# Kernel optimization log

Hardware: AMD Instinct MI355X
Metric: run time of the kernel (lower is better)

Reference implementation:

```python
import jax, jax.numpy as jnp
import numpy as np

BITS = 4
GROUP = 128
MAXQ = 2 ** BITS - 1  # 15 for asymmetric 4-bit


def round_ste(x):
    # straight-through rounding: round in fwd, identity in bwd
    return x + jax.lax.stop_gradient(jnp.round(x) - x)


def quant_weight(weight, v, min_scale, max_scale):
    """Groupwise asymmetric fake-quant (quantize + dequantize) of weight.

    weight: [O, I], v: [O, I] learnable rounding offsets,
    min_scale/max_scale: [O*I/GROUP] learnable min/max scales in [-1, 0].
    """
    O, I = weight.shape
    w = weight.reshape(-1, GROUP)          # [G, GROUP]
    vv = v.reshape(-1, GROUP)              # [G, GROUP]
    wmin_t = jnp.minimum(w.min(axis=1), 0.0)  # [G]
    wmax_t = jnp.maximum(w.max(axis=1), 0.0)  # [G]
    # forward clamps min/max scale into [-1, 0] before use
    wmin = wmin_t * (jnp.clip(min_scale, -1.0, 0.0) + 1.0)
    wmax = wmax_t * (jnp.clip(max_scale, -1.0, 0.0) + 1.0)
    degenerate = (wmin == 0.0) & (wmax == 0.0)
    wmin = jnp.where(degenerate, -1.0, wmin)
    wmax = jnp.where(degenerate, 1.0, wmax)
    # scale stored at fp16 precision (scale_dtype), then used in fp32 math
    scale = ((wmax - wmin) / MAXQ).astype(jnp.float16).astype(weight.dtype)  # [G]
    zp = round_ste(-wmin / scale)                                            # [G]
    int_w = round_ste(w / scale[:, None] + vv)                               # [G, GROUP]
    q = jnp.clip(int_w + zp[:, None], 0.0, float(MAXQ))
    wq = scale[:, None] * (q - zp[:, None])
    return wq.reshape(O, I)


def setup_inputs() -> dict:
    key = jax.random.key(0)
    k_x, k_w, k_b, k_v = jax.random.split(key, 4)
    O, I = 4096, 4096
    B, S = 2, 2048
    x = jax.random.normal(k_x, (B, S, I), dtype=jnp.float32)
    weight = jax.random.normal(k_w, (O, I), dtype=jnp.float32) * 0.02
    bias = jax.random.normal(k_b, (O,), dtype=jnp.float32) * 0.02
    value = jax.random.normal(k_v, (O, I), dtype=jnp.float32) * 0.1
    n_groups = O * I // GROUP
    min_scale = jnp.zeros((n_groups,), dtype=jnp.float32)
    max_scale = jnp.zeros((n_groups,), dtype=jnp.float32)
    return {"x": x, "weight": weight, "bias": bias, "value": value,
            "min_scale": min_scale, "max_scale": max_scale}


def reference(x, weight, bias, value, min_scale, max_scale):
    wq = quant_weight(weight, value, min_scale, max_scale)  # [O, I]
    # F.linear(x, weight_q, bias): x @ wq.T + bias
    return jnp.einsum('bsi,oi->bso', x, wq) + bias
```

## Files before the change

### kernel.cpp

```cpp
#include <hip/hip_runtime.h>
#include <hip/hip_bf16.h>
#include <hip/hip_fp16.h>
#include <stdint.h>

#define M_DIM 4096
#define N_DIM 4096
#define K_DIM 4096
#define GROUPSZ 128
#define MAXQ 15.0f

#define BM 256
#define BN 256
#define BK 64
#define T_TILES (K_DIM / BK)

typedef __attribute__((ext_vector_type(8))) short short8;
typedef __attribute__((ext_vector_type(4))) float f32x4;

__global__ __launch_bounds__(256) void quant_kernel(
    const float* __restrict__ weight, const float* __restrict__ value,
    const float* __restrict__ min_scale, const float* __restrict__ max_scale,
    __hip_bfloat16* __restrict__ wq)
{
    const int tid  = threadIdx.x;
    const int wave = tid >> 6;
    const int lane = tid & 63;
    const long g    = (long)blockIdx.x * 4 + wave;
    const long base = g * GROUPSZ + lane * 2;

    const float2 w = *(const float2*)(weight + base);
    const float2 v = *(const float2*)(value  + base);

    float mn = fminf(w.x, w.y);
    float mx = fmaxf(w.x, w.y);
#pragma unroll
    for (int off = 32; off >= 1; off >>= 1) {
        mn = fminf(mn, __shfl_xor(mn, off, 64));
        mx = fmaxf(mx, __shfl_xor(mx, off, 64));
    }
    mn = fminf(mn, 0.0f);
    mx = fmaxf(mx, 0.0f);

    const float ms = fminf(fmaxf(min_scale[g], -1.0f), 0.0f) + 1.0f;
    const float xs = fminf(fmaxf(max_scale[g], -1.0f), 0.0f) + 1.0f;
    float wmin = mn * ms;
    float wmax = mx * xs;
    if (wmin == 0.0f && wmax == 0.0f) { wmin = -1.0f; wmax = 1.0f; }

    const float scale = (float)(_Float16)((wmax - wmin) / MAXQ);
    const float zp    = rintf(-wmin / scale);

    const float q0 = fminf(fmaxf(rintf(w.x / scale + v.x) + zp, 0.0f), MAXQ);
    const float q1 = fminf(fmaxf(rintf(w.y / scale + v.y) + zp, 0.0f), MAXQ);
    const float o0 = scale * (q0 - zp);
    const float o1 = scale * (q1 - zp);

    __hip_bfloat162 o;
    o.x = __float2bfloat16(o0);
    o.y = __float2bfloat16(o1);
    *(__hip_bfloat162*)(wq + base) = o;
}

__global__ __launch_bounds__(256) void cast_kernel(
    const float* __restrict__ x, __hip_bfloat16* __restrict__ xb)
{
    const long i = ((long)blockIdx.x * 256 + threadIdx.x) * 8;
    const float4 a = *(const float4*)(x + i);
    const float4 b = *(const float4*)(x + i + 4);
    union { short8 s; __hip_bfloat16 h[8]; } u;
    u.h[0] = __float2bfloat16(a.x);
    u.h[1] = __float2bfloat16(a.y);
    u.h[2] = __float2bfloat16(a.z);
    u.h[3] = __float2bfloat16(a.w);
    u.h[4] = __float2bfloat16(b.x);
    u.h[5] = __float2bfloat16(b.y);
    u.h[6] = __float2bfloat16(b.z);
    u.h[7] = __float2bfloat16(b.w);
    *(short8*)(xb + i) = u.s;
}

__global__ __launch_bounds__(512, 2) void gemm_kernel(
    const __hip_bfloat16* __restrict__ A,
    const __hip_bfloat16* __restrict__ B,
    const float* __restrict__ bias,
    float* __restrict__ C)
{
    __shared__ __align__(16) char lds[131072];

    const int tid  = threadIdx.x;
    const int lane = tid & 63;
    const int wv   = tid >> 6;
    const int wm   = wv >> 2;
    const int wn   = wv & 3;

    const int bid = blockIdx.x;
    const int swz = (bid & 7) * (gridDim.x >> 3) + (bid >> 3);
    const int brow = (swz >> 4) * BM;
    const int bcol = (swz & 15) * BN;

    const int stg_r = tid >> 3;
    const int cc    = ((tid & 7) ^ (stg_r & 7)) * 8;

#define STAGE(XP, rowbase, h, tau, ldsbase)                                         \
    { _Pragma("unroll")                                                             \
      for (int inst = 0; inst < 2; ++inst) {                                        \
        const __hip_bfloat16* g = (XP) +                                            \
            (size_t)((rowbase) + (h) * 128 + inst * 64 + stg_r) * K_DIM +           \
            (tau) * 64 + cc;                                                        \
        __builtin_amdgcn_global_load_lds(                                           \
            (const __attribute__((address_space(1))) void*)g,                       \
            (__attribute__((address_space(3))) void*)(lds + (ldsbase) +             \
                (h) * 16384 + inst * 8192 + (wv << 10)),                            \
            16, 0, 0);                                                              \
      } }

#define STAGE_TILE(tau, bc)                                                         \
    STAGE(A, brow, 0, tau, (bc) * 32768);                                           \
    STAGE(A, brow, 1, tau, (bc) * 32768);                                           \
    STAGE(B, bcol, 0, tau, 65536 + (bc) * 32768);                                   \
    STAGE(B, bcol, 1, tau, 65536 + (bc) * 32768);

    const int ro = lane & 15;
    const int hi = lane >> 4;
    const int slot0 = ((0 + hi) ^ (ro & 7)) << 4;
    const int slot1 = ((4 + hi) ^ (ro & 7)) << 4;
    const int rbA = (wm * 128 + ro) * 128;
    const int rbB = (wn * 64  + ro) * 128;

    f32x4 acc[8][4] = {};

#define MFMA16(M0, X0, X1)                                                          \
    { _Pragma("unroll")                                                             \
      for (int n = 0; n < 4; ++n) {                                                 \
        acc[M0][n]     = __builtin_amdgcn_mfma_f32_16x16x32_bf16((X0)[0], bfr[n][0], acc[M0][n],     0, 0, 0); \
        acc[M0 + 1][n] = __builtin_amdgcn_mfma_f32_16x16x32_bf16((X1)[0], bfr[n][0], acc[M0 + 1][n], 0, 0, 0); \
      }                                                                             \
      _Pragma("unroll")                                                             \
      for (int n = 0; n < 4; ++n) {                                                 \
        acc[M0][n]     = __builtin_amdgcn_mfma_f32_16x16x32_bf16((X0)[1], bfr[n][1], acc[M0][n],     0, 0, 0); \
        acc[M0 + 1][n] = __builtin_amdgcn_mfma_f32_16x16x32_bf16((X1)[1], bfr[n][1], acc[M0 + 1][n], 0, 0, 0); \
      } }

#define LDA2(dst, m)                                                                \
    dst[0] = *(const short8*)(bA + (m) * 2048 + slot0);                             \
    dst[1] = *(const short8*)(bA + (m) * 2048 + slot1);

    STAGE_TILE(0, 0);
    STAGE_TILE(1, 1);

#pragma unroll 1
    for (int t = 0; t < T_TILES; ++t) {
        const int c = t & 1;
        const char* bA = lds + c * 32768 + rbA;
        const char* bB = lds + 65536 + c * 32768 + rbB;

        if (t < T_TILES - 1) { asm volatile("s_waitcnt vmcnt(8)" ::: "memory"); }
        else                 { asm volatile("s_waitcnt vmcnt(0)" ::: "memory"); }
        __builtin_amdgcn_s_barrier();

        short8 bfr[4][2];
        short8 a0[2][2], a1[2][2], a2[2][2], a3[2][2];

#pragma unroll
        for (int n = 0; n < 4; ++n) {
            bfr[n][0] = *(const short8*)(bB + n * 2048 + slot0);
            bfr[n][1] = *(const short8*)(bB + n * 2048 + slot1);
        }
        LDA2(a0[0], 0); LDA2(a0[1], 1);

        LDA2(a1[0], 2); LDA2(a1[1], 3);
        asm volatile("s_waitcnt lgkmcnt(4)" ::: "memory");
        __builtin_amdgcn_sched_barrier(0);
        __builtin_amdgcn_s_setprio(1);
        MFMA16(0, a0[0], a0[1]);
        __builtin_amdgcn_s_setprio(0);

        LDA2(a2[0], 4); LDA2(a2[1], 5);
        asm volatile("s_waitcnt lgkmcnt(4)" ::: "memory");
        __builtin_amdgcn_sched_barrier(0);
        __builtin_amdgcn_s_setprio(1);
        MFMA16(2, a1[0], a1[1]);
        __builtin_amdgcn_s_setprio(0);

        LDA2(a3[0], 6); LDA2(a3[1], 7);
        asm volatile("s_waitcnt lgkmcnt(4)" ::: "memory");
        __builtin_amdgcn_sched_barrier(0);
        __builtin_amdgcn_s_setprio(1);
        MFMA16(4, a2[0], a2[1]);
        __builtin_amdgcn_s_setprio(0);

        asm volatile("s_waitcnt lgkmcnt(0)" ::: "memory");
        __builtin_amdgcn_sched_barrier(0);
        __builtin_amdgcn_s_barrier();

        if (t + 2 < T_TILES) { STAGE_TILE(t + 2, c); }

        __builtin_amdgcn_s_setprio(1);
        MFMA16(6, a3[0], a3[1]);
        __builtin_amdgcn_s_setprio(0);
    }

    const int col   = lane & 15;
    const int rbase = hi * 4;
    float bv[4];
#pragma unroll
    for (int n = 0; n < 4; ++n)
        bv[n] = bias[bcol + wn * 64 + n * 16 + col];

#pragma unroll
    for (int m = 0; m < 8; ++m) {
        const int mrow = brow + wm * 128 + m * 16 + rbase;
#pragma unroll
        for (int r = 0; r < 4; ++r) {
            float* crow = C + (size_t)(mrow + r) * N_DIM + bcol + wn * 64 + col;
#pragma unroll
            for (int n = 0; n < 4; ++n)
                crow[n * 16] = acc[m][n][r] + bv[n];
        }
    }
#undef STAGE
#undef STAGE_TILE
#undef MFMA16
#undef LDA2
}

extern "C" void kernel_launch(void* const* d_in, const int* in_sizes, int n_in,
                              void* d_out, int out_size, void* d_ws, size_t ws_size,
                              hipStream_t stream) {
    const float* x         = (const float*)d_in[0];
    const float* weight    = (const float*)d_in[1];
    const float* bias      = (const float*)d_in[2];
    const float* value     = (const float*)d_in[3];
    const float* min_scale = (const float*)d_in[4];
    const float* max_scale = (const float*)d_in[5];
    float* out = (float*)d_out;

    __hip_bfloat16* xb  = (__hip_bfloat16*)d_ws;
    __hip_bfloat16* wqb = xb + (size_t)M_DIM * K_DIM;

    quant_kernel<<<(N_DIM * K_DIM / GROUPSZ) / 4, 256, 0, stream>>>(
        weight, value, min_scale, max_scale, wqb);
    cast_kernel<<<(M_DIM * K_DIM) / (256 * 8), 256, 0, stream>>>(x, xb);
    gemm_kernel<<<(M_DIM / BM) * (N_DIM / BN), 512, 0, stream>>>(xb, wqb, bias, out);
}
```

Measured before the change: 175.0 us.

## Restructure GEMM main loop to single-tile lookahead with register-prefetched fragments

The main loop now stages tile t+1 at the start of iteration t, instead of keeping two tiles in flight. At the end of each iteration it waits for all global loads, hits a barrier, and preloads the next tile's B fragments and first A fragments into registers. This removes the mid-iteration barrier and moves the LDS read of the first fragments off the critical path at the loop top. The cost is a shallower global-load prefetch, so load latency is hidden by only one iteration of MFMA work, and register pressure rises from the loop-carried fragments.

```diff
diff --git a/kernel.cpp b/kernel.cpp
--- a/kernel.cpp
+++ b/kernel.cpp
@@ -145,34 +145,37 @@
     dst[0] = *(const short8*)(bA + (m) * 2048 + slot0);                             \
     dst[1] = *(const short8*)(bA + (m) * 2048 + slot1);
 
+    short8 bfr[4][2];
+    short8 a0p[2][2];
+
     STAGE_TILE(0, 0);
-    STAGE_TILE(1, 1);
+    asm volatile("s_waitcnt vmcnt(0)" ::: "memory");
+    __builtin_amdgcn_s_barrier();
+    {
+        const char* bB = lds + 65536 + rbB;
+        const char* bA = lds + rbA;
+#pragma unroll
+        for (int n = 0; n < 4; ++n) {
+            bfr[n][0] = *(const short8*)(bB + n * 2048 + slot0);
+            bfr[n][1] = *(const short8*)(bB + n * 2048 + slot1);
+        }
+        LDA2(a0p[0], 0); LDA2(a0p[1], 1);
+    }
 
 #pragma unroll 1
     for (int t = 0; t < T_TILES; ++t) {
         const int c = t & 1;
         const char* bA = lds + c * 32768 + rbA;
-        const char* bB = lds + 65536 + c * 32768 + rbB;
-
-        if (t < T_TILES - 1) { asm volatile("s_waitcnt vmcnt(8)" ::: "memory"); }
-        else                 { asm volatile("s_waitcnt vmcnt(0)" ::: "memory"); }
-        __builtin_amdgcn_s_barrier();
-
-        short8 bfr[4][2];
-        short8 a0[2][2], a1[2][2], a2[2][2], a3[2][2];
-
-#pragma unroll
-        for (int n = 0; n < 4; ++n) {
-            bfr[n][0] = *(const short8*)(bB + n * 2048 + slot0);
-            bfr[n][1] = *(const short8*)(bB + n * 2048 + slot1);
-        }
-        LDA2(a0[0], 0); LDA2(a0[1], 1);
+
+        if (t + 1 < T_TILES) { STAGE_TILE(t + 1, c ^ 1); }
+
+        short8 a1[2][2], a2[2][2], a3[2][2];
 
         LDA2(a1[0], 2); LDA2(a1[1], 3);
         asm volatile("s_waitcnt lgkmcnt(4)" ::: "memory");
         __builtin_amdgcn_sched_barrier(0);
         __builtin_amdgcn_s_setprio(1);
-        MFMA16(0, a0[0], a0[1]);
+        MFMA16(0, a0p[0], a0p[1]);
         __builtin_amdgcn_s_setprio(0);
 
         LDA2(a2[0], 4); LDA2(a2[1], 5);
@@ -191,13 +194,24 @@
 
         asm volatile("s_waitcnt lgkmcnt(0)" ::: "memory");
         __builtin_amdgcn_sched_barrier(0);
-        __builtin_amdgcn_s_barrier();
-
-        if (t + 2 < T_TILES) { STAGE_TILE(t + 2, c); }
-
         __builtin_amdgcn_s_setprio(1);
         MFMA16(6, a3[0], a3[1]);
         __builtin_amdgcn_s_setprio(0);
+
+        if (t + 1 < T_TILES) {
+            asm volatile("s_waitcnt vmcnt(0)" ::: "memory");
+            __builtin_amdgcn_s_barrier();
+            const char* bBn = lds + 65536 + (c ^ 1) * 32768 + rbB;
+#pragma unroll
+            for (int n = 0; n < 4; ++n) {
+                bfr[n][0] = *(const short8*)(bBn + n * 2048 + slot0);
+                bfr[n][1] = *(const short8*)(bBn + n * 2048 + slot1);
+            }
+            {
+                const char* bA = lds + (c ^ 1) * 32768 + rbA;
+                LDA2(a0p[0], 0); LDA2(a0p[1], 1);
+            }
+        }
     }
 
     const int col   = lane & 15;
```

Result: faster. 170.3 us (-2.7%).

## Restructure GEMM main loop into one-tile-ahead prefetch with register-carried fragments

Applied to the files above, without the earlier changes.

The bf16 MFMA main loop is reworked. Global-to-LDS staging of the next K tile now starts at the top of each iteration, replacing the previous two-tile-deep prefetch. The first A/B fragments of the next tile are loaded into registers right after a vmcnt(0)+barrier, so LDS reads overlap the last MFMA block. MFMAs are regrouped into four 4x4 blocks split by K-half slot, with fragments double-buffered across phases. The aim is to hide LDS read latency behind MFMAs, at the cost of waiting for all global loads every iteration, which may expose memory latency.

```diff
diff --git a/kernel.cpp b/kernel.cpp
--- a/kernel.cpp
+++ b/kernel.cpp
@@ -129,74 +129,81 @@
 
     f32x4 acc[8][4] = {};
 
-#define MFMA16(M0, X0, X1)                                                          \
+#define MFMA_C(M0, AF, BF)                                                          \
     { _Pragma("unroll")                                                             \
       for (int n = 0; n < 4; ++n) {                                                 \
-        acc[M0][n]     = __builtin_amdgcn_mfma_f32_16x16x32_bf16((X0)[0], bfr[n][0], acc[M0][n],     0, 0, 0); \
-        acc[M0 + 1][n] = __builtin_amdgcn_mfma_f32_16x16x32_bf16((X1)[0], bfr[n][0], acc[M0 + 1][n], 0, 0, 0); \
-      }                                                                             \
-      _Pragma("unroll")                                                             \
-      for (int n = 0; n < 4; ++n) {                                                 \
-        acc[M0][n]     = __builtin_amdgcn_mfma_f32_16x16x32_bf16((X0)[1], bfr[n][1], acc[M0][n],     0, 0, 0); \
-        acc[M0 + 1][n] = __builtin_amdgcn_mfma_f32_16x16x32_bf16((X1)[1], bfr[n][1], acc[M0 + 1][n], 0, 0, 0); \
+        _Pragma("unroll")                                                           \
+        for (int mm = 0; mm < 4; ++mm)                                              \
+            acc[(M0) + mm][n] = __builtin_amdgcn_mfma_f32_16x16x32_bf16(            \
+                AF[mm], BF[n], acc[(M0) + mm][n], 0, 0, 0);                         \
       } }
 
-#define LDA2(dst, m)                                                                \
-    dst[0] = *(const short8*)(bA + (m) * 2048 + slot0);                             \
-    dst[1] = *(const short8*)(bA + (m) * 2048 + slot1);
+#define RDA4(dst, base, M0, S)                                                      \
+    dst[0] = *(const short8*)((base) + ((M0) + 0) * 2048 + (S));                    \
+    dst[1] = *(const short8*)((base) + ((M0) + 1) * 2048 + (S));                    \
+    dst[2] = *(const short8*)((base) + ((M0) + 2) * 2048 + (S));                    \
+    dst[3] = *(const short8*)((base) + ((M0) + 3) * 2048 + (S));
+
+#define RDB4(dst, base, S)                                                          \
+    dst[0] = *(const short8*)((base) + 0 * 2048 + (S));                             \
+    dst[1] = *(const short8*)((base) + 1 * 2048 + (S));                             \
+    dst[2] = *(const short8*)((base) + 2 * 2048 + (S));                             \
+    dst[3] = *(const short8*)((base) + 3 * 2048 + (S));
+
+    short8 bfr0[4], bfr1[4];
+    short8 afA[4], afB[4], afC[4], afD[4];
 
     STAGE_TILE(0, 0);
-    STAGE_TILE(1, 1);
+    asm volatile("s_waitcnt vmcnt(0)" ::: "memory");
+    __builtin_amdgcn_s_barrier();
+    RDA4(afA, lds + rbA, 0, slot0);
+    RDB4(bfr0, lds + 65536 + rbB, slot0);
 
 #pragma unroll 1
     for (int t = 0; t < T_TILES; ++t) {
         const int c = t & 1;
-        const char* bA = lds + c * 32768 + rbA;
-        const char* bB = lds + 65536 + c * 32768 + rbB;
-
-        if (t < T_TILES - 1) { asm volatile("s_waitcnt vmcnt(8)" ::: "memory"); }
-        else                 { asm volatile("s_waitcnt vmcnt(0)" ::: "memory"); }
-        __builtin_amdgcn_s_barrier();
-
-        short8 bfr[4][2];
-        short8 a0[2][2], a1[2][2], a2[2][2], a3[2][2];
-
-#pragma unroll
-        for (int n = 0; n < 4; ++n) {
-            bfr[n][0] = *(const short8*)(bB + n * 2048 + slot0);
-            bfr[n][1] = *(const short8*)(bB + n * 2048 + slot1);
+        const char* bA  = lds + c * 32768 + rbA;
+        const char* bB  = lds + 65536 + c * 32768 + rbB;
+        const char* bAn = lds + (c ^ 1) * 32768 + rbA;
+        const char* bBn = lds + 65536 + (c ^ 1) * 32768 + rbB;
+
+        if (t + 1 < T_TILES) { STAGE_TILE(t + 1, c ^ 1); }
+
+        RDA4(afB, bA, 4, slot0);
+        RDB4(bfr1, bB, slot1);
+        asm volatile("s_waitcnt lgkmcnt(8)" ::: "memory");
+        __builtin_amdgcn_sched_barrier(0);
+        __builtin_amdgcn_s_setprio(1);
+        MFMA_C(0, afA, bfr0);
+        __builtin_amdgcn_s_setprio(0);
+
+        RDA4(afC, bA, 0, slot1);
+        asm volatile("s_waitcnt lgkmcnt(8)" ::: "memory");
+        __builtin_amdgcn_sched_barrier(0);
+        __builtin_amdgcn_s_setprio(1);
+        MFMA_C(4, afB, bfr0);
+        __builtin_amdgcn_s_setprio(0);
+
+        RDA4(afD, bA, 4, slot1);
+        asm volatile("s_waitcnt lgkmcnt(4)" ::: "memory");
+        __builtin_amdgcn_sched_barrier(0);
+        __builtin_amdgcn_s_setprio(1);
+        MFMA_C(0, afC, bfr1);
+        __builtin_amdgcn_s_setprio(0);
+
+        asm volatile("s_waitcnt lgkmcnt(0)" ::: "memory");
+        __builtin_amdgcn_sched_barrier(0);
+
+        if (t + 1 < T_TILES) {
+            asm volatile("s_waitcnt vmcnt(0)" ::: "memory");
+            __builtin_amdgcn_s_barrier();
+            RDA4(afA, bAn, 0, slot0);
+            RDB4(bfr0, bBn, slot0);
+            __builtin_amdgcn_sched_barrier(0);
         }
-        LDA2(a0[0], 0); LDA2(a0[1], 1);
-
-        LDA2(a1[0], 2); LDA2(a1[1], 3);
-        asm volatile("s_waitcnt lgkmcnt(4)" ::: "memory");
-        __builtin_amdgcn_sched_barrier(0);
-        __builtin_amdgcn_s_setprio(1);
-        MFMA16(0, a0[0], a0[1]);
-        __builtin_amdgcn_s_setprio(0);
-
-        LDA2(a2[0], 4); LDA2(a2[1], 5);
-        asm volatile("s_waitcnt lgkmcnt(4)" ::: "memory");
-        __builtin_amdgcn_sched_barrier(0);
-        __builtin_amdgcn_s_setprio(1);
-        MFMA16(2, a1[0], a1[1]);
-        __builtin_amdgcn_s_setprio(0);
-
-        LDA2(a3[0], 6); LDA2(a3[1], 7);
-        asm volatile("s_waitcnt lgkmcnt(4)" ::: "memory");
-        __builtin_amdgcn_sched_barrier(0);
-        __builtin_amdgcn_s_setprio(1);
-        MFMA16(4, a2[0], a2[1]);
-        __builtin_amdgcn_s_setprio(0);
-
-        asm volatile("s_waitcnt lgkmcnt(0)" ::: "memory");
-        __builtin_amdgcn_sched_barrier(0);
-        __builtin_amdgcn_s_barrier();
-
-        if (t + 2 < T_TILES) { STAGE_TILE(t + 2, c); }
-
-        __builtin_amdgcn_s_setprio(1);
-        MFMA16(6, a3[0], a3[1]);
+
+        __builtin_amdgcn_s_setprio(1);
+        MFMA_C(4, afD, bfr1);
         __builtin_amdgcn_s_setprio(0);
     }
 
@@ -220,8 +227,9 @@
     }
 #undef STAGE
 #undef STAGE_TILE
-#undef MFMA16
-#undef LDA2
+#undef MFMA_C
+#undef RDA4
+#undef RDB4
 }
 
 extern "C" void kernel_launch(void* const* d_in, const int* in_sizes, int n_in,
```

New measurement: 167.9 us. 4.1% less time.
